# Optimization experiments

Measured on AMD Instinct MI355X. Metric: run time of the kernel, lower is better.

The kernel has to match this reference:

```python
import jax, jax.numpy as jnp
import numpy as np

B, T, D = 32, 1024, 1024
H = D // 2  # hidden per direction


def setup_inputs() -> dict:
    key = jax.random.key(0)
    ks = jax.random.split(key, 8)
    s_in = 1.0 / np.sqrt(D).astype(np.float32)
    s_h = 1.0 / np.sqrt(H).astype(np.float32)
    return {
        "x": jax.random.normal(ks[0], (B, T, D), jnp.float32),
        "Wx_f": jax.random.normal(ks[1], (D, 4 * H), jnp.float32) * s_in,
        "Wh_f": jax.random.normal(ks[2], (H, 4 * H), jnp.float32) * s_h,
        "b_f": jnp.zeros((4 * H,), jnp.float32),
        "Wx_b": jax.random.normal(ks[3], (D, 4 * H), jnp.float32) * s_in,
        "Wh_b": jax.random.normal(ks[4], (H, 4 * H), jnp.float32) * s_h,
        "b_b": jnp.zeros((4 * H,), jnp.float32),
        "W_fc": jax.random.normal(ks[5], (2 * H, 1), jnp.float32) * (1.0 / np.sqrt(2 * H).astype(np.float32)),
        "b_fc": jnp.zeros((1,), jnp.float32),
    }


def _lstm_dir(x_tm, Wx, Wh, b):
    # x_tm: [T, B, D] time-major. Standard LSTM, gate order (i, f, g, o).
    Bn = x_tm.shape[1]
    Hh = Wh.shape[0]
    # Precompute input projections for all timesteps in one big GEMM.
    xg = jnp.einsum('tbd,dg->tbg', x_tm, Wx) + b  # [T, B, 4H]

    def step(carry, xg_t):
        h, c = carry
        g = xg_t + h @ Wh  # [B, 4H]
        i, f, gg, o = jnp.split(g, 4, axis=-1)
        i = jax.nn.sigmoid(i)
        f = jax.nn.sigmoid(f)
        gg = jnp.tanh(gg)
        o = jax.nn.sigmoid(o)
        c = f * c + i * gg
        h = o * jnp.tanh(c)
        return (h, c), h

    init = (jnp.zeros((Bn, Hh), x_tm.dtype), jnp.zeros((Bn, Hh), x_tm.dtype))
    _, hs = jax.lax.scan(step, init, xg)
    return hs  # [T, B, H]


def reference(x, Wx_f, Wh_f, b_f, Wx_b, Wh_b, b_b, W_fc, b_fc):
    xt = jnp.transpose(x, (1, 0, 2))  # [T, B, D]
    h_fwd = _lstm_dir(xt, Wx_f, Wh_f, b_f)              # [T, B, H]
    h_bwd = _lstm_dir(xt[::-1], Wx_b, Wh_b, b_b)[::-1]  # [T, B, H]
    h = jnp.concatenate([h_fwd, h_bwd], axis=-1)        # [T, B, 2H]
    logits = jnp.einsum('tbh,h->tb', h, W_fc[:, 0]) + b_fc[0]
    out = jax.nn.sigmoid(logits)                        # [T, B]
    return jnp.transpose(out)                           # [B, T]
```

## Files before the change

kernel.cpp:

```cpp
#include <hip/hip_runtime.h>
#include <hip/hip_bf16.h>
#include <cstdint>
#include <cstddef>

#define TT 1024
#define BB 32
#define DD 1024
#define HH 512
#define GG 2048

#define POISON_U64 0xFC00FC00FC00FC00ull

typedef _Float16 f16x8 __attribute__((ext_vector_type(8)));
typedef _Float16 f16x4 __attribute__((ext_vector_type(4)));
typedef float    f32x4 __attribute__((ext_vector_type(4)));

__device__ __forceinline__ float sigm(float x) { return 1.0f / (1.0f + __expf(-x)); }
__device__ __forceinline__ float tanh_fast(float x) { return 2.0f / (1.0f + __expf(-2.0f * x)) - 1.0f; }

__global__ __launch_bounds__(256) void init_kernel(unsigned long long* __restrict__ hr) {
    const int i = blockIdx.x * 256 + threadIdx.x;
    const int slot = (i >> 11) & 3;
    hr[i] = (slot == 0) ? 0ull : POISON_U64;
}

__global__ __launch_bounds__(256) void transpose_f16(const float* __restrict__ in,
                                                     _Float16* __restrict__ out,
                                                     int K, int N) {
    __shared__ float tile[32][33];
    const int tx = threadIdx.x & 31, ty = threadIdx.x >> 5;
    const int n0 = blockIdx.x * 32, k0 = blockIdx.y * 32;
#pragma unroll
    for (int j = 0; j < 4; j++)
        tile[ty + 8 * j][tx] = in[(size_t)(k0 + ty + 8 * j) * N + n0 + tx];
    __syncthreads();
#pragma unroll
    for (int j = 0; j < 4; j++)
        out[(size_t)(n0 + ty + 8 * j) * K + k0 + tx] = (_Float16)tile[tx][ty + 8 * j];
}

__global__ __launch_bounds__(256) void gemm_xg(const float* __restrict__ x,
                                               const _Float16* __restrict__ WxT_f,
                                               const float* __restrict__ b_f,
                                               const _Float16* __restrict__ WxT_b,
                                               const float* __restrict__ b_b,
                                               _Float16* __restrict__ xg_f,
                                               _Float16* __restrict__ xg_b) {
    const int dir = blockIdx.z;
    const _Float16* __restrict__ WxT = dir ? WxT_b : WxT_f;
    const float* __restrict__ bias = dir ? b_b : b_f;
    _Float16* __restrict__ out = dir ? xg_b : xg_f;

    const int c0 = blockIdx.x * 32;
    const int m0 = blockIdx.y * 128;

    __shared__ __align__(16) unsigned char smem[40960];
    _Float16* A_lds = (_Float16*)smem;
    _Float16* B_lds = (_Float16*)(smem + 18432);
    _Float16* stage = (_Float16*)smem;

    const int tid = threadIdx.x;
    const int wave = tid >> 6;
    const int lane = tid & 63;
    const int jn = lane & 15;
    const int quad = lane >> 4;

    f32x4 acc[2][8] = {};

    for (int k0 = 0; k0 < DD; k0 += 64) {
        {
            const int kq = tid & 15;
            const int mq = tid >> 4;
#pragma unroll
            for (int i = 0; i < 8; i++) {
                const int m = mq + 16 * i;
                const int gm = m0 + m;
                const int t = gm >> 5;
                const int b = gm & 31;
                const float4 v = *(const float4*)(x + ((size_t)b * TT + t) * DD + k0 + kq * 4);
                f16x4 f;
                f.x = (_Float16)v.x; f.y = (_Float16)v.y;
                f.z = (_Float16)v.z; f.w = (_Float16)v.w;
                *(f16x4*)(A_lds + m * 72 + kq * 4) = f;
            }
        }
        {
            const int kq = tid & 7;
            const int nq = tid >> 3;
#pragma unroll
            for (int i = 0; i < 4; i++) {
                const int nl = nq + 32 * i;
                const int g = nl >> 5;
                const int c = nl & 31;
                f16x8 w = *(const f16x8*)(WxT + (size_t)(g * 512 + c0 + c) * DD + k0 + kq * 8);
                *(f16x8*)(B_lds + nl * 72 + kq * 8) = w;
            }
        }
        __syncthreads();
#pragma unroll
        for (int kc = 0; kc < 64; kc += 32) {
            const f16x8 a0 = *(const f16x8*)(A_lds + (wave * 32 + jn) * 72 + kc + quad * 8);
            const f16x8 a1 = *(const f16x8*)(A_lds + (wave * 32 + 16 + jn) * 72 + kc + quad * 8);
#pragma unroll
            for (int nt = 0; nt < 8; nt++) {
                const f16x8 bb = *(const f16x8*)(B_lds + (nt * 16 + jn) * 72 + kc + quad * 8);
                acc[0][nt] = __builtin_amdgcn_mfma_f32_16x16x32_f16(a0, bb, acc[0][nt], 0, 0, 0);
                acc[1][nt] = __builtin_amdgcn_mfma_f32_16x16x32_f16(a1, bb, acc[1][nt], 0, 0, 0);
            }
        }
        __syncthreads();
    }

    float bv[8];
#pragma unroll
    for (int nt = 0; nt < 8; nt++)
        bv[nt] = bias[(nt >> 1) * 512 + c0 + (nt & 1) * 16 + jn];

    const int lsi = dir ? (3 - wave) : wave;
#pragma unroll
    for (int mt = 0; mt < 2; mt++) {
#pragma unroll
        for (int r = 0; r < 4; r++) {
            const int b = mt * 16 + quad * 4 + r;
#pragma unroll
            for (int nt = 0; nt < 8; nt++) {
                const int c = (nt & 1) * 16 + jn;
                stage[c * 520 + b * 16 + lsi * 4 + (nt >> 1)] =
                    (_Float16)(acc[mt][nt][r] + bv[nt]);
            }
        }
    }
    __syncthreads();

    const int sidx0 = dir ? (1020 - blockIdx.y * 4) : (blockIdx.y * 4);
    const int sc = sidx0 >> 3;
    const int si0 = sidx0 & 7;
#pragma unroll
    for (int it = 0; it < 4; it++) {
        const int p = it * 256 + tid;
        const int c = p & 31;
        const int b = p >> 5;
        const int cglob = c0 + c;
        const int blk = cglob >> 4;
        const int jl = cglob & 15;
        const f16x8* srcp = (const f16x8*)(stage + c * 520 + b * 16);
        const size_t obase =
            ((((size_t)(blk * 32 + b) * 16 + jl) * 128 + sc) * 8 + si0) * 4;
        *(f16x8*)(out + obase) = srcp[0];
        *(f16x8*)(out + obase + 8) = srcp[1];
    }
}

__global__ __launch_bounds__(512) void lstm_persist(
    const _Float16* __restrict__ xg_f,
    const _Float16* __restrict__ xg_b,
    const _Float16* __restrict__ WhT_f,
    const _Float16* __restrict__ WhT_b,
    const float* __restrict__ wfc,
    unsigned long long* __restrict__ hring,
    _Float16* __restrict__ part) {

    __shared__ __align__(16) _Float16 h_lds[16 * 520];
    __shared__ float red[4 * 16 * 33];

    const int tid = threadIdx.x;
    const int bid = blockIdx.x;
    const int dir = bid >> 5;
    const int grp = (bid >> 4) & 1;
    const int blk = bid & 15;

    const _Float16* __restrict__ xg = dir ? xg_b : xg_f;
    const _Float16* __restrict__ WhT = dir ? WhT_b : WhT_f;
    unsigned long long* hp = hring + ((size_t)(dir * 2 + grp)) * 8192;

    const int lane = tid & 63;
    const int wave = tid >> 6;
    const int g = wave >> 1;
    const int half = wave & 1;
    const int jl16 = lane & 15;
    const int quad = lane >> 4;

    f16x8 bfrag[16];
    {
        const _Float16* wcol = WhT + (size_t)(g * 512 + blk * 32 + half * 16 + jl16) * HH;
#pragma unroll
        for (int i = 0; i < 16; i++)
            bfrag[i] = *(const f16x8*)(wcol + i * 32 + quad * 8);
    }

    const int gb = tid >> 5;
    const int gc = tid & 31;
    float c_reg = 0.0f;
    const float wfc_reg = wfc[dir * 512 + blk * 32 + gc];

    unsigned long long* hl64 = (unsigned long long*)h_lds;
    const int blk32 = blk * 2 + (gc >> 4);
    const int b_glob = grp * 16 + gb;
    const _Float16* xbase =
        xg + (((size_t)(blk32 * 32 + b_glob) * 16 + (gc & 15)) * 128) * 32;

    const int prod_idx = gb * 128 + blk * 8 + (gc >> 2);
    const bool is_prod = ((gc & 3) == 0);

    f16x8 xcur[4];
    {
        const f16x8* src0 = (const f16x8*)(xbase);
#pragma unroll
        for (int q = 0; q < 4; q++) xcur[q] = src0[q];
    }

    for (int sc = 0; sc < 128; sc++) {
        f16x8 xnxt[4];
        if (sc < 127) {
            const f16x8* srcn = (const f16x8*)(xbase + (sc + 1) * 32);
#pragma unroll
            for (int q = 0; q < 4; q++) xnxt[q] = srcn[q];
        }

#pragma unroll
        for (int si = 0; si < 8; si++) {
            const int s = sc * 8 + si;
            const int t = dir ? (1023 - s) : s;

            if (s >= 2 && is_prod)
                __hip_atomic_store(hp + (size_t)((s - 2) & 3) * 2048 + prod_idx,
                                   POISON_U64, __ATOMIC_RELAXED,
                                   __HIP_MEMORY_SCOPE_AGENT);

            {
                const unsigned long long* __restrict__ src =
                    hp + (size_t)(s & 3) * 2048;
                unsigned int pend = 0xFu;
                int guard = 0;
                do {
                    unsigned long long v[4];
#pragma unroll
                    for (int q = 0; q < 4; q++)
                        if (pend & (1u << q))
                            v[q] = __hip_atomic_load(src + q * 512 + tid,
                                                     __ATOMIC_RELAXED,
                                                     __HIP_MEMORY_SCOPE_AGENT);
                    unsigned int got = 0;
#pragma unroll
                    for (int q = 0; q < 4; q++) {
                        if ((pend & (1u << q)) &&
                            ((unsigned int)v[q] & 0xFFFFu) != 0xFC00u) {
                            const int idx = q * 512 + tid;
                            hl64[(idx >> 7) * 130 + (idx & 127)] = v[q];
                            got |= (1u << q);
                        }
                    }
                    pend &= ~got;
                    if (pend) {
                        if (got == 0) __builtin_amdgcn_s_sleep(1);
                        if (++guard > (1 << 18)) break;
                    }
                } while (pend);
            }
            __syncthreads();

            {
                f32x4 a0 = {0.f, 0.f, 0.f, 0.f};
                f32x4 a1 = {0.f, 0.f, 0.f, 0.f};
                f32x4 a2 = {0.f, 0.f, 0.f, 0.f};
                f32x4 a3 = {0.f, 0.f, 0.f, 0.f};
                const _Float16* hrow = h_lds + jl16 * 520 + quad * 8;
#pragma unroll
                for (int i = 0; i < 4; i++) {
                    const f16x8 h0 = *(const f16x8*)(hrow + 32 * i);
                    const f16x8 h1 = *(const f16x8*)(hrow + 32 * (i + 4));
                    const f16x8 h2 = *(const f16x8*)(hrow + 32 * (i + 8));
                    const f16x8 h3 = *(const f16x8*)(hrow + 32 * (i + 12));
                    a0 = __builtin_amdgcn_mfma_f32_16x16x32_f16(h0, bfrag[i],      a0, 0, 0, 0);
                    a1 = __builtin_amdgcn_mfma_f32_16x16x32_f16(h1, bfrag[i + 4],  a1, 0, 0, 0);
                    a2 = __builtin_amdgcn_mfma_f32_16x16x32_f16(h2, bfrag[i + 8],  a2, 0, 0, 0);
                    a3 = __builtin_amdgcn_mfma_f32_16x16x32_f16(h3, bfrag[i + 12], a3, 0, 0, 0);
                }
                const f32x4 acc = (a0 + a1) + (a2 + a3);
#pragma unroll
                for (int r = 0; r < 4; r++)
                    red[(g * 16 + quad * 4 + r) * 33 + half * 16 + jl16] = acc[r];
            }
            __syncthreads();

            {
                const float p0 = red[(0 * 16 + gb) * 33 + gc] + (float)xcur[si >> 1][(si & 1) * 4 + 0];
                const float p1 = red[(1 * 16 + gb) * 33 + gc] + (float)xcur[si >> 1][(si & 1) * 4 + 1];
                const float p2 = red[(2 * 16 + gb) * 33 + gc] + (float)xcur[si >> 1][(si & 1) * 4 + 2];
                const float p3 = red[(3 * 16 + gb) * 33 + gc] + (float)xcur[si >> 1][(si & 1) * 4 + 3];

                const float gi = sigm(p0);
                const float gf = sigm(p1);
                const float gc_ = tanh_fast(p2);
                const float go = sigm(p3);
                c_reg = gf * c_reg + gi * gc_;
                const float hval = go * tanh_fast(c_reg);

                const float hnb = __shfl_xor(hval, 1);
                union { struct { _Float16 lo, hi; } h; unsigned int u; } cvt;
                cvt.h.lo = (_Float16)hval;
                cvt.h.hi = (_Float16)hnb;
                const unsigned int pair2 = __shfl_xor(cvt.u, 2);
                if (is_prod) {
                    const unsigned long long pv =
                        ((unsigned long long)pair2 << 32) | (unsigned long long)cvt.u;
                    __hip_atomic_store(hp + (size_t)((s + 1) & 3) * 2048 + prod_idx, pv,
                                       __ATOMIC_RELAXED, __HIP_MEMORY_SCOPE_AGENT);
                }
                float contrib = hval * wfc_reg;
                contrib += __shfl_xor(contrib, 1);
                contrib += __shfl_xor(contrib, 2);
                contrib += __shfl_xor(contrib, 4);
                contrib += __shfl_xor(contrib, 8);
                contrib += __shfl_xor(contrib, 16);
                if (gc == 0)
                    part[(size_t)(t * 32 + b_glob) * 32 + dir * 16 + blk] = (_Float16)contrib;
            }
        }

        if (sc < 127) {
#pragma unroll
            for (int q = 0; q < 4; q++) xcur[q] = xnxt[q];
        }
    }
}

__global__ __launch_bounds__(256) void fc_final(const _Float16* __restrict__ part,
                                                const float* __restrict__ b_fc,
                                                float* __restrict__ out) {
    const int i = blockIdx.x * 256 + threadIdx.x;
    const int b = i >> 10;
    const int t = i & 1023;
    const f16x8* p = (const f16x8*)(part + (size_t)(t * 32 + b) * 32);
    float acc = b_fc[0];
#pragma unroll
    for (int q = 0; q < 4; q++) {
        const f16x8 v = p[q];
#pragma unroll
        for (int e = 0; e < 8; e++) acc += (float)v[e];
    }
    out[i] = sigm(acc);
}

extern "C" void kernel_launch(void* const* d_in, const int* in_sizes, int n_in,
                              void* d_out, int out_size, void* d_ws, size_t ws_size,
                              hipStream_t stream) {
    const float* x    = (const float*)d_in[0];
    const float* Wx_f = (const float*)d_in[1];
    const float* Wh_f = (const float*)d_in[2];
    const float* b_f  = (const float*)d_in[3];
    const float* Wx_b = (const float*)d_in[4];
    const float* Wh_b = (const float*)d_in[5];
    const float* b_b  = (const float*)d_in[6];
    const float* W_fc = (const float*)d_in[7];
    const float* b_fc = (const float*)d_in[8];
    float* out = (float*)d_out;

    const size_t XG       = 134217728ULL;
    const size_t WXT_OFF  = 2 * XG;
    const size_t WHT_OFF  = WXT_OFF + 2 * 4194304ULL;
    const size_t need     = WHT_OFF + 2 * 2097152ULL;
    if (ws_size < need) return;

    uint8_t* ws = (uint8_t*)d_ws;
    _Float16* xg_f = (_Float16*)ws;
    _Float16* xg_b = (_Float16*)(ws + XG);
    _Float16* WxT_f = (_Float16*)(ws + WXT_OFF);
    _Float16* WxT_b = (_Float16*)(ws + WXT_OFF + 4194304ULL);
    _Float16* WhT_f = (_Float16*)(ws + WHT_OFF);
    _Float16* WhT_b = (_Float16*)(ws + WHT_OFF + 2097152ULL);
    _Float16* part  = (_Float16*)(ws + WXT_OFF);
    unsigned long long* hring =
        (unsigned long long*)(ws + WXT_OFF + 4194304ULL);

    transpose_f16<<<dim3(64, 32), 256, 0, stream>>>(Wx_f, WxT_f, 1024, 2048);
    transpose_f16<<<dim3(64, 32), 256, 0, stream>>>(Wx_b, WxT_b, 1024, 2048);
    transpose_f16<<<dim3(64, 16), 256, 0, stream>>>(Wh_f, WhT_f, 512, 2048);
    transpose_f16<<<dim3(64, 16), 256, 0, stream>>>(Wh_b, WhT_b, 512, 2048);

    gemm_xg<<<dim3(16, 256, 2), 256, 0, stream>>>(
        x, WxT_f, b_f, WxT_b, b_b, xg_f, xg_b);

    init_kernel<<<128, 256, 0, stream>>>(hring);

    lstm_persist<<<64, 512, 0, stream>>>(
        xg_f, xg_b, WhT_f, WhT_b, W_fc, hring, part);

    fc_final<<<(BB * TT) / 256, 256, 0, stream>>>(part, b_fc, out);
}
```

Measured before the change: 3.372 ms.

## Repartition LSTM recurrence into 8 column blocks by 4 batch groups

Changes the persistent LSTM work split from 16 hidden-column blocks × 2 batch groups per direction to 8 column blocks × 4 batch groups. Each block now owns 64 hidden columns for 8 batch rows, using two N-tiles of MFMA with double the weight fragments in registers, and reads only half as much h from the ring buffer per step. The goal is to shrink the per-step cross-block exchange and polling traffic. In exchange, MFMA work per block grows with half the M rows wasted (only 8 of 16 rows valid), and register pressure goes up from the doubled bfrag.

```diff
diff --git a/kernel.cpp b/kernel.cpp
--- a/kernel.cpp
+++ b/kernel.cpp
@@ -20,7 +20,7 @@
 
 __global__ __launch_bounds__(256) void init_kernel(unsigned long long* __restrict__ hr) {
     const int i = blockIdx.x * 256 + threadIdx.x;
-    const int slot = (i >> 11) & 3;
+    const int slot = (i >> 10) & 3;
     hr[i] = (slot == 0) ? 0ull : POISON_U64;
 }
 
@@ -151,7 +151,7 @@
     }
 }
 
-__global__ __launch_bounds__(512) void lstm_persist(
+__global__ __launch_bounds__(512, 2) void lstm_persist(
     const _Float16* __restrict__ xg_f,
     const _Float16* __restrict__ xg_b,
     const _Float16* __restrict__ WhT_f,
@@ -161,46 +161,50 @@
     _Float16* __restrict__ part) {
 
     __shared__ __align__(16) _Float16 h_lds[16 * 520];
-    __shared__ float red[4 * 16 * 33];
+    __shared__ float red[4 * 8 * 66];
 
     const int tid = threadIdx.x;
     const int bid = blockIdx.x;
     const int dir = bid >> 5;
-    const int grp = (bid >> 4) & 1;
-    const int blk = bid & 15;
+    const int grp = (bid >> 3) & 3;
+    const int blk = bid & 7;
 
     const _Float16* __restrict__ xg = dir ? xg_b : xg_f;
     const _Float16* __restrict__ WhT = dir ? WhT_b : WhT_f;
-    unsigned long long* hp = hring + ((size_t)(dir * 2 + grp)) * 8192;
+    unsigned long long* hp = hring + ((size_t)(dir * 4 + grp)) * 4096;
 
     const int lane = tid & 63;
     const int wave = tid >> 6;
     const int g = wave >> 1;
-    const int half = wave & 1;
+    const int chalf = wave & 1;
     const int jl16 = lane & 15;
     const int quad = lane >> 4;
 
-    f16x8 bfrag[16];
-    {
-        const _Float16* wcol = WhT + (size_t)(g * 512 + blk * 32 + half * 16 + jl16) * HH;
+    f16x8 bfrag[2][16];
+#pragma unroll
+    for (int nt = 0; nt < 2; nt++) {
+        const _Float16* wcol =
+            WhT + (size_t)(g * 512 + blk * 64 + chalf * 32 + nt * 16 + jl16) * HH;
 #pragma unroll
         for (int i = 0; i < 16; i++)
-            bfrag[i] = *(const f16x8*)(wcol + i * 32 + quad * 8);
-    }
-
-    const int gb = tid >> 5;
-    const int gc = tid & 31;
+            bfrag[nt][i] = *(const f16x8*)(wcol + i * 32 + quad * 8);
+    }
+
+    const int gb = tid >> 6;
+    const int gc = tid & 63;
     float c_reg = 0.0f;
-    const float wfc_reg = wfc[dir * 512 + blk * 32 + gc];
+    const float wfc_reg = wfc[dir * 512 + blk * 64 + gc];
 
     unsigned long long* hl64 = (unsigned long long*)h_lds;
-    const int blk32 = blk * 2 + (gc >> 4);
-    const int b_glob = grp * 16 + gb;
+    const int blk32 = blk * 4 + (gc >> 4);
+    const int b_glob = grp * 8 + gb;
     const _Float16* xbase =
         xg + (((size_t)(blk32 * 32 + b_glob) * 16 + (gc & 15)) * 128) * 32;
 
-    const int prod_idx = gb * 128 + blk * 8 + (gc >> 2);
+    const int prod_idx = gb * 128 + blk * 16 + (gc >> 2);
     const bool is_prod = ((gc & 3) == 0);
+
+    for (int i = tid; i < 8 * 130; i += 512) hl64[8 * 130 + i] = 0ull;
 
     f16x8 xcur[4];
     {
@@ -223,32 +227,31 @@
             const int t = dir ? (1023 - s) : s;
 
             if (s >= 2 && is_prod)
-                __hip_atomic_store(hp + (size_t)((s - 2) & 3) * 2048 + prod_idx,
+                __hip_atomic_store(hp + (size_t)((s - 2) & 3) * 1024 + prod_idx,
                                    POISON_U64, __ATOMIC_RELAXED,
                                    __HIP_MEMORY_SCOPE_AGENT);
 
             {
                 const unsigned long long* __restrict__ src =
-                    hp + (size_t)(s & 3) * 2048;
-                unsigned int pend = 0xFu;
+                    hp + (size_t)(s & 3) * 1024;
+                unsigned int pend = 0x3u;
                 int guard = 0;
                 do {
-                    unsigned long long v[4];
-#pragma unroll
-                    for (int q = 0; q < 4; q++)
-                        if (pend & (1u << q))
-                            v[q] = __hip_atomic_load(src + q * 512 + tid,
-                                                     __ATOMIC_RELAXED,
-                                                     __HIP_MEMORY_SCOPE_AGENT);
+                    unsigned long long v[2];
+                    if (pend & 1u)
+                        v[0] = __hip_atomic_load(src + tid, __ATOMIC_RELAXED,
+                                                 __HIP_MEMORY_SCOPE_AGENT);
+                    if (pend & 2u)
+                        v[1] = __hip_atomic_load(src + 512 + tid, __ATOMIC_RELAXED,
+                                                 __HIP_MEMORY_SCOPE_AGENT);
                     unsigned int got = 0;
-#pragma unroll
-                    for (int q = 0; q < 4; q++) {
-                        if ((pend & (1u << q)) &&
-                            ((unsigned int)v[q] & 0xFFFFu) != 0xFC00u) {
-                            const int idx = q * 512 + tid;
-                            hl64[(idx >> 7) * 130 + (idx & 127)] = v[q];
-                            got |= (1u << q);
-                        }
+                    if ((pend & 1u) && ((unsigned int)v[0] & 0xFFFFu) != 0xFC00u) {
+                        hl64[(tid >> 7) * 130 + (tid & 127)] = v[0];
+                        got |= 1u;
+                    }
+                    if ((pend & 2u) && ((unsigned int)v[1] & 0xFFFFu) != 0xFC00u) {
+                        hl64[(4 + (tid >> 7)) * 130 + (tid & 127)] = v[1];
+                        got |= 2u;
                     }
                     pend &= ~got;
                     if (pend) {
@@ -260,10 +263,7 @@
             __syncthreads();
 
             {
-                f32x4 a0 = {0.f, 0.f, 0.f, 0.f};
-                f32x4 a1 = {0.f, 0.f, 0.f, 0.f};
-                f32x4 a2 = {0.f, 0.f, 0.f, 0.f};
-                f32x4 a3 = {0.f, 0.f, 0.f, 0.f};
+                f32x4 acc[2][4] = {};
                 const _Float16* hrow = h_lds + jl16 * 520 + quad * 8;
 #pragma unroll
                 for (int i = 0; i < 4; i++) {
@@ -271,23 +271,31 @@
                     const f16x8 h1 = *(const f16x8*)(hrow + 32 * (i + 4));
                     const f16x8 h2 = *(const f16x8*)(hrow + 32 * (i + 8));
                     const f16x8 h3 = *(const f16x8*)(hrow + 32 * (i + 12));
-                    a0 = __builtin_amdgcn_mfma_f32_16x16x32_f16(h0, bfrag[i],      a0, 0, 0, 0);
-                    a1 = __builtin_amdgcn_mfma_f32_16x16x32_f16(h1, bfrag[i + 4],  a1, 0, 0, 0);
-                    a2 = __builtin_amdgcn_mfma_f32_16x16x32_f16(h2, bfrag[i + 8],  a2, 0, 0, 0);
-                    a3 = __builtin_amdgcn_mfma_f32_16x16x32_f16(h3, bfrag[i + 12], a3, 0, 0, 0);
+#pragma unroll
+                    for (int nt = 0; nt < 2; nt++) {
+                        acc[nt][0] = __builtin_amdgcn_mfma_f32_16x16x32_f16(h0, bfrag[nt][i],      acc[nt][0], 0, 0, 0);
+                        acc[nt][1] = __builtin_amdgcn_mfma_f32_16x16x32_f16(h1, bfrag[nt][i + 4],  acc[nt][1], 0, 0, 0);
+                        acc[nt][2] = __builtin_amdgcn_mfma_f32_16x16x32_f16(h2, bfrag[nt][i + 8],  acc[nt][2], 0, 0, 0);
+                        acc[nt][3] = __builtin_amdgcn_mfma_f32_16x16x32_f16(h3, bfrag[nt][i + 12], acc[nt][3], 0, 0, 0);
+                    }
                 }
-                const f32x4 acc = (a0 + a1) + (a2 + a3);
-#pragma unroll
-                for (int r = 0; r < 4; r++)
-                    red[(g * 16 + quad * 4 + r) * 33 + half * 16 + jl16] = acc[r];
+                if (quad < 2) {
+#pragma unroll
+                    for (int nt = 0; nt < 2; nt++) {
+                        const f32x4 a = (acc[nt][0] + acc[nt][1]) + (acc[nt][2] + acc[nt][3]);
+#pragma unroll
+                        for (int r = 0; r < 4; r++)
+                            red[(g * 8 + quad * 4 + r) * 66 + chalf * 32 + nt * 16 + jl16] = a[r];
+                    }
+                }
             }
             __syncthreads();
 
             {
-                const float p0 = red[(0 * 16 + gb) * 33 + gc] + (float)xcur[si >> 1][(si & 1) * 4 + 0];
-                const float p1 = red[(1 * 16 + gb) * 33 + gc] + (float)xcur[si >> 1][(si & 1) * 4 + 1];
-                const float p2 = red[(2 * 16 + gb) * 33 + gc] + (float)xcur[si >> 1][(si & 1) * 4 + 2];
-                const float p3 = red[(3 * 16 + gb) * 33 + gc] + (float)xcur[si >> 1][(si & 1) * 4 + 3];
+                const float p0 = red[(0 * 8 + gb) * 66 + gc] + (float)xcur[si >> 1][(si & 1) * 4 + 0];
+                const float p1 = red[(1 * 8 + gb) * 66 + gc] + (float)xcur[si >> 1][(si & 1) * 4 + 1];
+                const float p2 = red[(2 * 8 + gb) * 66 + gc] + (float)xcur[si >> 1][(si & 1) * 4 + 2];
+                const float p3 = red[(3 * 8 + gb) * 66 + gc] + (float)xcur[si >> 1][(si & 1) * 4 + 3];
 
                 const float gi = sigm(p0);
                 const float gf = sigm(p1);
@@ -304,7 +312,7 @@
                 if (is_prod) {
                     const unsigned long long pv =
                         ((unsigned long long)pair2 << 32) | (unsigned long long)cvt.u;
-                    __hip_atomic_store(hp + (size_t)((s + 1) & 3) * 2048 + prod_idx, pv,
+                    __hip_atomic_store(hp + (size_t)((s + 1) & 3) * 1024 + prod_idx, pv,
                                        __ATOMIC_RELAXED, __HIP_MEMORY_SCOPE_AGENT);
                 }
                 float contrib = hval * wfc_reg;
@@ -313,8 +321,9 @@
                 contrib += __shfl_xor(contrib, 4);
                 contrib += __shfl_xor(contrib, 8);
                 contrib += __shfl_xor(contrib, 16);
+                contrib += __shfl_xor(contrib, 32);
                 if (gc == 0)
-                    part[(size_t)(t * 32 + b_glob) * 32 + dir * 16 + blk] = (_Float16)contrib;
+                    part[(size_t)(t * 32 + b_glob) * 16 + dir * 8 + blk] = (_Float16)contrib;
             }
         }
 
@@ -331,10 +340,10 @@
     const int i = blockIdx.x * 256 + threadIdx.x;
     const int b = i >> 10;
     const int t = i & 1023;
-    const f16x8* p = (const f16x8*)(part + (size_t)(t * 32 + b) * 32);
+    const f16x8* p = (const f16x8*)(part + (size_t)(t * 32 + b) * 16);
     float acc = b_fc[0];
 #pragma unroll
-    for (int q = 0; q < 4; q++) {
+    for (int q = 0; q < 2; q++) {
         const f16x8 v = p[q];
 #pragma unroll
         for (int e = 0; e < 8; e++) acc += (float)v[e];
```

Result: slower. 3.622 ms (+7.4%).

## Merge forward and backward LSTM directions into one persistent block

Applied to the files above, without the earlier changes.

Each persistent block now holds the recurrent weights of both directions and alternates forward and backward timesteps, halving the grid from 64 to 32 blocks. The intent is to have one direction's cross-block h exchange overlap with the other's compute and to use fewer CUs. The cost is doubled register use for weight fragments and x prefetch, with spill risk under the added occupancy hint. Each block's per-step work and barriers are also serialized across both directions.

```diff
diff --git a/kernel.cpp b/kernel.cpp
--- a/kernel.cpp
+++ b/kernel.cpp
@@ -151,7 +151,7 @@
     }
 }
 
-__global__ __launch_bounds__(512) void lstm_persist(
+__global__ __launch_bounds__(512, 2) void lstm_persist(
     const _Float16* __restrict__ xg_f,
     const _Float16* __restrict__ xg_b,
     const _Float16* __restrict__ WhT_f,
@@ -165,13 +165,8 @@
 
     const int tid = threadIdx.x;
     const int bid = blockIdx.x;
-    const int dir = bid >> 5;
-    const int grp = (bid >> 4) & 1;
+    const int grp = bid >> 4;
     const int blk = bid & 15;
-
-    const _Float16* __restrict__ xg = dir ? xg_b : xg_f;
-    const _Float16* __restrict__ WhT = dir ? WhT_b : WhT_f;
-    unsigned long long* hp = hring + ((size_t)(dir * 2 + grp)) * 8192;
 
     const int lane = tid & 63;
     const int wave = tid >> 6;
@@ -180,147 +175,165 @@
     const int jl16 = lane & 15;
     const int quad = lane >> 4;
 
-    f16x8 bfrag[16];
-    {
+    f16x8 bfrag[2][16];
+#pragma unroll
+    for (int d = 0; d < 2; d++) {
+        const _Float16* __restrict__ WhT = d ? WhT_b : WhT_f;
         const _Float16* wcol = WhT + (size_t)(g * 512 + blk * 32 + half * 16 + jl16) * HH;
 #pragma unroll
         for (int i = 0; i < 16; i++)
-            bfrag[i] = *(const f16x8*)(wcol + i * 32 + quad * 8);
+            bfrag[d][i] = *(const f16x8*)(wcol + i * 32 + quad * 8);
     }
 
     const int gb = tid >> 5;
     const int gc = tid & 31;
-    float c_reg = 0.0f;
-    const float wfc_reg = wfc[dir * 512 + blk * 32 + gc];
+    float c_reg[2] = {0.0f, 0.0f};
+    float wfc_reg[2];
+    wfc_reg[0] = wfc[0 * 512 + blk * 32 + gc];
+    wfc_reg[1] = wfc[1 * 512 + blk * 32 + gc];
 
     unsigned long long* hl64 = (unsigned long long*)h_lds;
     const int blk32 = blk * 2 + (gc >> 4);
     const int b_glob = grp * 16 + gb;
-    const _Float16* xbase =
-        xg + (((size_t)(blk32 * 32 + b_glob) * 16 + (gc & 15)) * 128) * 32;
+    const _Float16* xbase[2];
+    xbase[0] = xg_f + (((size_t)(blk32 * 32 + b_glob) * 16 + (gc & 15)) * 128) * 32;
+    xbase[1] = xg_b + (((size_t)(blk32 * 32 + b_glob) * 16 + (gc & 15)) * 128) * 32;
+    unsigned long long* hp[2];
+    hp[0] = hring + ((size_t)(0 * 2 + grp)) * 8192;
+    hp[1] = hring + ((size_t)(1 * 2 + grp)) * 8192;
 
     const int prod_idx = gb * 128 + blk * 8 + (gc >> 2);
     const bool is_prod = ((gc & 3) == 0);
 
-    f16x8 xcur[4];
-    {
-        const f16x8* src0 = (const f16x8*)(xbase);
-#pragma unroll
-        for (int q = 0; q < 4; q++) xcur[q] = src0[q];
+    f16x8 xcur[2][4];
+#pragma unroll
+    for (int d = 0; d < 2; d++) {
+        const f16x8* src0 = (const f16x8*)(xbase[d]);
+#pragma unroll
+        for (int q = 0; q < 4; q++) xcur[d][q] = src0[q];
     }
 
     for (int sc = 0; sc < 128; sc++) {
-        f16x8 xnxt[4];
+        f16x8 xnxt[2][4];
         if (sc < 127) {
-            const f16x8* srcn = (const f16x8*)(xbase + (sc + 1) * 32);
-#pragma unroll
-            for (int q = 0; q < 4; q++) xnxt[q] = srcn[q];
+#pragma unroll
+            for (int d = 0; d < 2; d++) {
+                const f16x8* srcn = (const f16x8*)(xbase[d] + (sc + 1) * 32);
+#pragma unroll
+                for (int q = 0; q < 4; q++) xnxt[d][q] = srcn[q];
+            }
         }
 
 #pragma unroll
         for (int si = 0; si < 8; si++) {
             const int s = sc * 8 + si;
-            const int t = dir ? (1023 - s) : s;
-
-            if (s >= 2 && is_prod)
-                __hip_atomic_store(hp + (size_t)((s - 2) & 3) * 2048 + prod_idx,
-                                   POISON_U64, __ATOMIC_RELAXED,
-                                   __HIP_MEMORY_SCOPE_AGENT);
-
-            {
-                const unsigned long long* __restrict__ src =
-                    hp + (size_t)(s & 3) * 2048;
-                unsigned int pend = 0xFu;
-                int guard = 0;
-                do {
-                    unsigned long long v[4];
-#pragma unroll
-                    for (int q = 0; q < 4; q++)
-                        if (pend & (1u << q))
-                            v[q] = __hip_atomic_load(src + q * 512 + tid,
-                                                     __ATOMIC_RELAXED,
-                                                     __HIP_MEMORY_SCOPE_AGENT);
-                    unsigned int got = 0;
-#pragma unroll
-                    for (int q = 0; q < 4; q++) {
-                        if ((pend & (1u << q)) &&
-                            ((unsigned int)v[q] & 0xFFFFu) != 0xFC00u) {
-                            const int idx = q * 512 + tid;
-                            hl64[(idx >> 7) * 130 + (idx & 127)] = v[q];
-                            got |= (1u << q);
+
+#pragma unroll
+            for (int d = 0; d < 2; d++) {
+                const int t = d ? (1023 - s) : s;
+
+                if (s >= 2 && is_prod)
+                    __hip_atomic_store(hp[d] + (size_t)((s - 2) & 3) * 2048 + prod_idx,
+                                       POISON_U64, __ATOMIC_RELAXED,
+                                       __HIP_MEMORY_SCOPE_AGENT);
+
+                {
+                    const unsigned long long* __restrict__ src =
+                        hp[d] + (size_t)(s & 3) * 2048;
+                    unsigned int pend = 0xFu;
+                    int guard = 0;
+                    do {
+                        unsigned long long v[4];
+#pragma unroll
+                        for (int q = 0; q < 4; q++)
+                            if (pend & (1u << q))
+                                v[q] = __hip_atomic_load(src + q * 512 + tid,
+                                                         __ATOMIC_RELAXED,
+                                                         __HIP_MEMORY_SCOPE_AGENT);
+                        unsigned int got = 0;
+#pragma unroll
+                        for (int q = 0; q < 4; q++) {
+                            if ((pend & (1u << q)) &&
+                                ((unsigned int)v[q] & 0xFFFFu) != 0xFC00u) {
+                                const int idx = q * 512 + tid;
+                                hl64[(idx >> 7) * 130 + (idx & 127)] = v[q];
+                                got |= (1u << q);
+                            }
                         }
+                        pend &= ~got;
+                        if (pend) {
+                            if (got == 0) __builtin_amdgcn_s_sleep(1);
+                            if (++guard > (1 << 18)) break;
+                        }
+                    } while (pend);
+                }
+                __syncthreads();
+
+                {
+                    f32x4 a0 = {0.f, 0.f, 0.f, 0.f};
+                    f32x4 a1 = {0.f, 0.f, 0.f, 0.f};
+                    f32x4 a2 = {0.f, 0.f, 0.f, 0.f};
+                    f32x4 a3 = {0.f, 0.f, 0.f, 0.f};
+                    const _Float16* hrow = h_lds + jl16 * 520 + quad * 8;
+#pragma unroll
+                    for (int i = 0; i < 4; i++) {
+                        const f16x8 h0 = *(const f16x8*)(hrow + 32 * i);
+                        const f16x8 h1 = *(const f16x8*)(hrow + 32 * (i + 4));
+                        const f16x8 h2 = *(const f16x8*)(hrow + 32 * (i + 8));
+                        const f16x8 h3 = *(const f16x8*)(hrow + 32 * (i + 12));
+                        a0 = __builtin_amdgcn_mfma_f32_16x16x32_f16(h0, bfrag[d][i],      a0, 0, 0, 0);
+                        a1 = __builtin_amdgcn_mfma_f32_16x16x32_f16(h1, bfrag[d][i + 4],  a1, 0, 0, 0);
+                        a2 = __builtin_amdgcn_mfma_f32_16x16x32_f16(h2, bfrag[d][i + 8],  a2, 0, 0, 0);
+                        a3 = __builtin_amdgcn_mfma_f32_16x16x32_f16(h3, bfrag[d][i + 12], a3, 0, 0, 0);
                     }
-                    pend &= ~got;
-                    if (pend) {
-                        if (got == 0) __builtin_amdgcn_s_sleep(1);
-                        if (++guard > (1 << 18)) break;
+                    const f32x4 acc = (a0 + a1) + (a2 + a3);
+#pragma unroll
+                    for (int r = 0; r < 4; r++)
+                        red[(g * 16 + quad * 4 + r) * 33 + half * 16 + jl16] = acc[r];
+                }
+                __syncthreads();
+
+                {
+                    const float p0 = red[(0 * 16 + gb) * 33 + gc] + (float)xcur[d][si >> 1][(si & 1) * 4 + 0];
+                    const float p1 = red[(1 * 16 + gb) * 33 + gc] + (float)xcur[d][si >> 1][(si & 1) * 4 + 1];
+                    const float p2 = red[(2 * 16 + gb) * 33 + gc] + (float)xcur[d][si >> 1][(si & 1) * 4 + 2];
+                    const float p3 = red[(3 * 16 + gb) * 33 + gc] + (float)xcur[d][si >> 1][(si & 1) * 4 + 3];
+
+                    const float gi = sigm(p0);
+                    const float gf = sigm(p1);
+                    const float gc_ = tanh_fast(p2);
+                    const float go = sigm(p3);
+                    c_reg[d] = gf * c_reg[d] + gi * gc_;
+                    const float hval = go * tanh_fast(c_reg[d]);
+
+                    const float hnb = __shfl_xor(hval, 1);
+                    union { struct { _Float16 lo, hi; } h; unsigned int u; } cvt;
+                    cvt.h.lo = (_Float16)hval;
+                    cvt.h.hi = (_Float16)hnb;
+                    const unsigned int pair2 = __shfl_xor(cvt.u, 2);
+                    if (is_prod) {
+                        const unsigned long long pv =
+                            ((unsigned long long)pair2 << 32) | (unsigned long long)cvt.u;
+                        __hip_atomic_store(hp[d] + (size_t)((s + 1) & 3) * 2048 + prod_idx, pv,
+                                           __ATOMIC_RELAXED, __HIP_MEMORY_SCOPE_AGENT);
                     }
-                } while (pend);
-            }
-            __syncthreads();
-
-            {
-                f32x4 a0 = {0.f, 0.f, 0.f, 0.f};
-                f32x4 a1 = {0.f, 0.f, 0.f, 0.f};
-                f32x4 a2 = {0.f, 0.f, 0.f, 0.f};
-                f32x4 a3 = {0.f, 0.f, 0.f, 0.f};
-                const _Float16* hrow = h_lds + jl16 * 520 + quad * 8;
-#pragma unroll
-                for (int i = 0; i < 4; i++) {
-                    const f16x8 h0 = *(const f16x8*)(hrow + 32 * i);
-                    const f16x8 h1 = *(const f16x8*)(hrow + 32 * (i + 4));
-                    const f16x8 h2 = *(const f16x8*)(hrow + 32 * (i + 8));
-                    const f16x8 h3 = *(const f16x8*)(hrow + 32 * (i + 12));
-                    a0 = __builtin_amdgcn_mfma_f32_16x16x32_f16(h0, bfrag[i],      a0, 0, 0, 0);
-                    a1 = __builtin_amdgcn_mfma_f32_16x16x32_f16(h1, bfrag[i + 4],  a1, 0, 0, 0);
-                    a2 = __builtin_amdgcn_mfma_f32_16x16x32_f16(h2, bfrag[i + 8],  a2, 0, 0, 0);
-                    a3 = __builtin_amdgcn_mfma_f32_16x16x32_f16(h3, bfrag[i + 12], a3, 0, 0, 0);
+                    float contrib = hval * wfc_reg[d];
+                    contrib += __shfl_xor(contrib, 1);
+                    contrib += __shfl_xor(contrib, 2);
+                    contrib += __shfl_xor(contrib, 4);
+                    contrib += __shfl_xor(contrib, 8);
+                    contrib += __shfl_xor(contrib, 16);
+                    if (gc == 0)
+                        part[(size_t)(t * 32 + b_glob) * 32 + d * 16 + blk] = (_Float16)contrib;
                 }
-                const f32x4 acc = (a0 + a1) + (a2 + a3);
-#pragma unroll
-                for (int r = 0; r < 4; r++)
-                    red[(g * 16 + quad * 4 + r) * 33 + half * 16 + jl16] = acc[r];
-            }
-            __syncthreads();
-
-            {
-                const float p0 = red[(0 * 16 + gb) * 33 + gc] + (float)xcur[si >> 1][(si & 1) * 4 + 0];
-                const float p1 = red[(1 * 16 + gb) * 33 + gc] + (float)xcur[si >> 1][(si & 1) * 4 + 1];
-                const float p2 = red[(2 * 16 + gb) * 33 + gc] + (float)xcur[si >> 1][(si & 1) * 4 + 2];
-                const float p3 = red[(3 * 16 + gb) * 33 + gc] + (float)xcur[si >> 1][(si & 1) * 4 + 3];
-
-                const float gi = sigm(p0);
-                const float gf = sigm(p1);
-                const float gc_ = tanh_fast(p2);
-                const float go = sigm(p3);
-                c_reg = gf * c_reg + gi * gc_;
-                const float hval = go * tanh_fast(c_reg);
-
-                const float hnb = __shfl_xor(hval, 1);
-                union { struct { _Float16 lo, hi; } h; unsigned int u; } cvt;
-                cvt.h.lo = (_Float16)hval;
-                cvt.h.hi = (_Float16)hnb;
-                const unsigned int pair2 = __shfl_xor(cvt.u, 2);
-                if (is_prod) {
-                    const unsigned long long pv =
-                        ((unsigned long long)pair2 << 32) | (unsigned long long)cvt.u;
-                    __hip_atomic_store(hp + (size_t)((s + 1) & 3) * 2048 + prod_idx, pv,
-                                       __ATOMIC_RELAXED, __HIP_MEMORY_SCOPE_AGENT);
-                }
-                float contrib = hval * wfc_reg;
-                contrib += __shfl_xor(contrib, 1);
-                contrib += __shfl_xor(contrib, 2);
-                contrib += __shfl_xor(contrib, 4);
-                contrib += __shfl_xor(contrib, 8);
-                contrib += __shfl_xor(contrib, 16);
-                if (gc == 0)
-                    part[(size_t)(t * 32 + b_glob) * 32 + dir * 16 + blk] = (_Float16)contrib;
             }
         }
 
         if (sc < 127) {
 #pragma unroll
-            for (int q = 0; q < 4; q++) xcur[q] = xnxt[q];
+            for (int d = 0; d < 2; d++)
+#pragma unroll
+                for (int q = 0; q < 4; q++) xcur[d][q] = xnxt[d][q];
         }
     }
 }
@@ -383,7 +396,7 @@
 
     init_kernel<<<128, 256, 0, stream>>>(hring);
 
-    lstm_persist<<<64, 512, 0, stream>>>(
+    lstm_persist<<<32, 512, 0, stream>>>(
         xg_f, xg_b, WhT_f, WhT_b, W_fc, hring, part);
 
     fc_final<<<(BB * TT) / 256, 256, 0, stream>>>(part, b_fc, out);
```

Measured after the change: 8.115 ms. 141% more time.
